# Optimization experiments

Measured on AMD Instinct MI355X. Metric: run time of the kernel, lower is better.

The kernel has to match this reference:

```python
import jax, jax.numpy as jnp
import numpy as np

B, N, HID, NH = 16, 200, 64, 2
D = HID // NH
EPS = 1e-12
LOG_EPS = 1e-24


def setup_inputs() -> dict:
    key = jax.random.key(0)
    ks = jax.random.split(key, 24)
    r = lambda k, shp, s=1.0: (jax.random.normal(k, shp, dtype=jnp.float32) * s)
    inp = {
        "input_tensor": r(ks[0], (B, N, HID), 0.5),
        "attention_mask": jnp.zeros((B, 1, N, N), jnp.float32),
        "absolute_pos_K": r(ks[1], (B, N, HID), 0.5),
        "absolute_pos_V": r(ks[2], (B, N, HID), 0.5),
        "time_matrix_emb_K": r(ks[3], (B, N, N, HID), 0.1),
        "time_matrix_emb_V": r(ks[4], (B, N, N, HID), 0.1),
        # learned params (torch nn.Linear convention: y = x @ W.T + b)
        "Wq": r(ks[5], (HID, HID), 0.02), "bq": jnp.zeros((HID,), jnp.float32),
        "Wk": r(ks[6], (HID, HID), 0.02), "bk": jnp.zeros((HID,), jnp.float32),
        "Wv": r(ks[7], (HID, HID), 0.02), "bv": jnp.zeros((HID,), jnp.float32),
        "Wd": r(ks[8], (HID, HID), 0.02), "bd": jnp.zeros((HID,), jnp.float32),
        "order_w": r(ks[9], (2 * D,), 0.02), "order_b": jnp.zeros((1,), jnp.float32),
        "dist_w": r(ks[10], (2 * D,), 0.02), "dist_b": jnp.zeros((1,), jnp.float32),
        "scalar": r(ks[11], (1,)),
        "ln_g": jnp.ones((HID,), jnp.float32), "ln_b": jnp.zeros((HID,), jnp.float32),
    }
    return inp


def _split_heads(x):  # [B,N,HID] -> [B,NH,N,D]
    return x.reshape(B, N, NH, D).transpose(0, 2, 1, 3)


def reference(input_tensor, attention_mask, absolute_pos_K, absolute_pos_V,
              time_matrix_emb_K, time_matrix_emb_V,
              Wq, bq, Wk, bk, Wv, bv, Wd, bd,
              order_w, order_b, dist_w, dist_b, scalar, ln_g, ln_b):
    q = _split_heads(input_tensor @ Wq.T + bq)   # [B,H,N,D]
    k = _split_heads(input_tensor @ Wk.T + bk)
    v = _split_heads(input_tensor @ Wv.T + bv)
    pk = _split_heads(absolute_pos_K)
    pv = _split_heads(absolute_pos_V)
    tk = time_matrix_emb_K.reshape(B, N, N, NH, D).transpose(0, 3, 1, 2, 4)  # [B,H,N,N,D]
    tv = time_matrix_emb_V.reshape(B, N, N, NH, D).transpose(0, 3, 1, 2, 4)

    scores = jnp.einsum('bhid,bhjd->bhij', q, k)
    scores = scores + jnp.einsum('bhid,bhjd->bhij', q, pk)
    scores = scores + jnp.einsum('bhijd,bhid->bhij', tk, q)

    # order term: order_affine(cat(q_i, k_j)) decomposes as q_i.w1 + k_j.w2 + b,
    # so we never materialize the [B,H,N,N,2D] q_k tensor.
    logit_o = (jnp.einsum('bhid,d->bhi', q, order_w[:D])[..., :, None]
               + jnp.einsum('bhjd,d->bhj', k, order_w[D:])[..., None, :]
               + order_b[0])
    pr_order = jax.nn.sigmoid(logit_o)
    gd_order = jnp.triu(jnp.ones((N, N), jnp.float32), 1)  # 1 where j > i
    err_order = (jnp.log(pr_order + LOG_EPS) * gd_order
                 + jnp.log(1.0 - pr_order + LOG_EPS) * (1.0 - gd_order))

    # distance term (same decomposition)
    pr_dist = (jnp.einsum('bhid,d->bhi', q, dist_w[:D])[..., :, None]
               + jnp.einsum('bhjd,d->bhj', k, dist_w[D:])[..., None, :]
               + dist_b[0])
    idx = jnp.arange(N)
    gd_dist = jnp.log(jnp.abs(idx[None, :] - idx[:, None]).astype(jnp.float32) + 1.0)
    err_dist = -jnp.square(gd_dist - pr_dist) * jnp.square(scalar[0]) * 0.5

    scores = (scores + err_order + err_dist) / np.sqrt(D).astype(np.float32)
    scores = scores + attention_mask
    probs = jax.nn.softmax(scores, axis=-1)  # dropout is identity in eval mode

    ctx = (jnp.einsum('bhij,bhjd->bhid', probs, v)
           + jnp.einsum('bhij,bhjd->bhid', probs, pv)
           + jnp.einsum('bhij,bhijd->bhid', probs, tv))
    ctx = ctx.transpose(0, 2, 1, 3).reshape(B, N, HID)

    h = ctx @ Wd.T + bd + input_tensor
    mu = h.mean(-1, keepdims=True)
    var = jnp.square(h - mu).mean(-1, keepdims=True)
    return (h - mu) / jnp.sqrt(var + EPS) * ln_g + ln_b
```

## Files before the change

kernel.cpp:

```cpp
#include <hip/hip_runtime.h>
#include <math.h>

#define B 16
#define N 200
#define HID 64
#define NH 2
#define D 32
#define EPSF 1e-12f
#define LOG_EPSF 1e-24f

#define RSQRT_D 0.17677669529663687f

__global__ __launch_bounds__(256) void k_proj(
    const float* __restrict__ x,
    const float* __restrict__ pk,
    const float* __restrict__ pv,
    const float* __restrict__ Wq, const float* __restrict__ bq,
    const float* __restrict__ Wk, const float* __restrict__ bk,
    const float* __restrict__ Wv, const float* __restrict__ bv,
    const float* __restrict__ order_w, const float* __restrict__ dist_w,
    float* __restrict__ q,
    float* __restrict__ kp,
    float* __restrict__ vp,
    float* __restrict__ qo, float* __restrict__ ko,
    float* __restrict__ qd, float* __restrict__ kd)
{
    __shared__ float sX[4][HID];
    const int tid = threadIdx.x;
    const int sub = tid >> 6;
    const int o   = tid & 63;
    const int row = blockIdx.x * 4 + sub;

    sX[sub][o] = x[row * HID + o];
    __syncthreads();

    float qv = bq[o], kv = bk[o], vv = bv[o];
    #pragma unroll 8
    for (int c = 0; c < HID; ++c) {
        const float xv = sX[sub][c];
        qv = fmaf(xv, Wq[o * HID + c], qv);
        kv = fmaf(xv, Wk[o * HID + c], kv);
        vv = fmaf(xv, Wv[o * HID + c], vv);
    }
    q [row * HID + o] = qv;
    kp[row * HID + o] = kv + pk[row * HID + o];
    vp[row * HID + o] = vv + pv[row * HID + o];

    const int d = o & 31;
    float qov = qv * order_w[d];
    float kov = kv * order_w[D + d];
    float qdv = qv * dist_w[d];
    float kdv = kv * dist_w[D + d];
    #pragma unroll
    for (int m = 16; m >= 1; m >>= 1) {
        qov += __shfl_xor(qov, m);
        kov += __shfl_xor(kov, m);
        qdv += __shfl_xor(qdv, m);
        kdv += __shfl_xor(kdv, m);
    }
    if (d == 0) {
        const int bb = row / N;
        const int ii = row - bb * N;
        const int h  = o >> 5;
        const int idx = (bb * NH + h) * N + ii;
        qo[idx] = qov;  ko[idx] = kov;
        qd[idx] = qdv;  kd[idx] = kdv;
    }
}

__global__ __launch_bounds__(64) void k_attn(
    const float* __restrict__ q, const float* __restrict__ kp,
    const float* __restrict__ vp,
    const float* __restrict__ tk,
    const float* __restrict__ tv,
    const float* __restrict__ amask,
    const float* __restrict__ qo, const float* __restrict__ ko,
    const float* __restrict__ qd, const float* __restrict__ kd,
    const float* __restrict__ order_b, const float* __restrict__ dist_b,
    const float* __restrict__ scalar,
    float* __restrict__ ctx)
{
    __shared__ float S_aux[256];
    __shared__ float S_dot[256];

    const int lane = threadIdx.x;
    const int g    = lane >> 3;
    const int c    = lane & 7;
    const int bid  = blockIdx.x;
    const int bh   = bid / N;
    const int i    = bid - bh * N;
    const int b    = bh >> 1;
    const int h    = bh & 1;
    const int bi   = b * N + i;

    const float4 qf = ((const float4*)(q + (size_t)bi * HID + h * D))[c];

    const float qoi = qo[bh * N + i];
    const float qdi = qd[bh * N + i];
    const float ob  = order_b[0];
    const float db  = dist_b[0];
    const float sc  = scalar[0];
    const float sc2h = 0.5f * sc * sc;

    const float* kpb = kp + (size_t)b * N * HID + h * D;
    const float* tkb = tk + (size_t)bi * N * HID + h * D;
    const float* vpb = vp + (size_t)b * N * HID + h * D;
    const float* tvb = tv + (size_t)bi * N * HID + h * D;
    const float* mb  = amask + (size_t)bi * N;
    const float* kob = ko + (size_t)bh * N;
    const float* kdb = kd + (size_t)bh * N;

    #pragma unroll
    for (int r = 0; r < 4; ++r) {
        const int j = r * 64 + lane;
        if (j < N) {
            const float lo = qoi + kob[j] + ob;
            const float xs = (j > i) ? -lo : lo;
            const float eo = -log1pf(expf(xs));
            const float pd = qdi + kdb[j] + db;
            const float gd = logf((float)(j > i ? j - i : i - j) + 1.0f);
            const float dv = gd - pd;
            S_aux[j] = (eo - sc2h * dv * dv) * RSQRT_D + mb[j];
        }
    }

    #pragma unroll 5
    for (int it = 0; it < 25; ++it) {
        const int j = it * 8 + g;
        const float4 kv  = ((const float4*)(kpb + (size_t)j * HID))[c];
        const float4 tkv = ((const float4*)(tkb + (size_t)j * HID))[c];
        float part = qf.x * (kv.x + tkv.x) + qf.y * (kv.y + tkv.y)
                   + qf.z * (kv.z + tkv.z) + qf.w * (kv.w + tkv.w);
        part += __shfl_xor(part, 1);
        part += __shfl_xor(part, 2);
        part += __shfl_xor(part, 4);
        if (c == 0) S_dot[j] = part * RSQRT_D;
    }
    asm volatile("s_waitcnt lgkmcnt(0)" ::: "memory");

    const float s0 = S_aux[lane]       + S_dot[lane];
    const float s1 = S_aux[lane + 64]  + S_dot[lane + 64];
    const float s2 = S_aux[lane + 128] + S_dot[lane + 128];
    const float s3 = (lane < 8) ? (S_aux[lane + 192] + S_dot[lane + 192]) : -INFINITY;
    float m = fmaxf(fmaxf(s0, s1), fmaxf(s2, s3));
    #pragma unroll
    for (int k = 32; k >= 1; k >>= 1) m = fmaxf(m, __shfl_xor(m, k));
    const float e0 = expf(s0 - m);
    const float e1 = expf(s1 - m);
    const float e2 = expf(s2 - m);
    const float e3 = (lane < 8) ? expf(s3 - m) : 0.0f;
    float t = e0 + e1 + e2 + e3;
    #pragma unroll
    for (int k = 32; k >= 1; k >>= 1) t += __shfl_xor(t, k);
    const float rinv = 1.0f / t;
    S_aux[lane]       = e0 * rinv;
    S_aux[lane + 64]  = e1 * rinv;
    S_aux[lane + 128] = e2 * rinv;
    if (lane < 8) S_aux[lane + 192] = e3 * rinv;
    asm volatile("s_waitcnt lgkmcnt(0)" ::: "memory");

    float4 r4 = make_float4(0.f, 0.f, 0.f, 0.f);
    #pragma unroll 5
    for (int it = 0; it < 25; ++it) {
        const int j = it * 8 + g;
        const float p = S_aux[j];
        const float4 vv  = ((const float4*)(vpb + (size_t)j * HID))[c];
        const float4 tvv = ((const float4*)(tvb + (size_t)j * HID))[c];
        r4.x += p * (vv.x + tvv.x);
        r4.y += p * (vv.y + tvv.y);
        r4.z += p * (vv.z + tvv.z);
        r4.w += p * (vv.w + tvv.w);
    }
    #pragma unroll
    for (int k = 8; k <= 32; k <<= 1) {
        r4.x += __shfl_xor(r4.x, k);
        r4.y += __shfl_xor(r4.y, k);
        r4.z += __shfl_xor(r4.z, k);
        r4.w += __shfl_xor(r4.w, k);
    }
    if (g == 0)
        ((float4*)(ctx + (size_t)bi * HID + h * D))[c] = r4;
}

__global__ __launch_bounds__(256) void k_out(
    const float* __restrict__ ctx, const float* __restrict__ x,
    const float* __restrict__ Wd, const float* __restrict__ bd,
    const float* __restrict__ ln_g, const float* __restrict__ ln_b,
    float* __restrict__ out)
{
    __shared__ float sC[4][HID];
    const int tid = threadIdx.x;
    const int sub = tid >> 6;
    const int o   = tid & 63;
    const int row = blockIdx.x * 4 + sub;

    sC[sub][o] = ctx[row * HID + o];
    __syncthreads();

    float hv = bd[o] + x[row * HID + o];
    #pragma unroll 8
    for (int c = 0; c < HID; ++c)
        hv = fmaf(sC[sub][c], Wd[o * HID + c], hv);

    float sum = hv;
    #pragma unroll
    for (int m = 32; m >= 1; m >>= 1) sum += __shfl_xor(sum, m);
    const float mu = sum * (1.0f / 64.0f);
    const float dv = hv - mu;
    float vs = dv * dv;
    #pragma unroll
    for (int m = 32; m >= 1; m >>= 1) vs += __shfl_xor(vs, m);
    const float var = vs * (1.0f / 64.0f);

    out[row * HID + o] = dv * rsqrtf(var + EPSF) * ln_g[o] + ln_b[o];
}

extern "C" void kernel_launch(void* const* d_in, const int* in_sizes, int n_in,
                              void* d_out, int out_size, void* d_ws, size_t ws_size,
                              hipStream_t stream) {
    const float* x     = (const float*)d_in[0];
    const float* amask = (const float*)d_in[1];
    const float* apk   = (const float*)d_in[2];
    const float* apv   = (const float*)d_in[3];
    const float* tk    = (const float*)d_in[4];
    const float* tv    = (const float*)d_in[5];
    const float* Wq    = (const float*)d_in[6];
    const float* bq    = (const float*)d_in[7];
    const float* Wk    = (const float*)d_in[8];
    const float* bk    = (const float*)d_in[9];
    const float* Wv    = (const float*)d_in[10];
    const float* bv    = (const float*)d_in[11];
    const float* Wd    = (const float*)d_in[12];
    const float* bd    = (const float*)d_in[13];
    const float* order_w = (const float*)d_in[14];
    const float* order_b = (const float*)d_in[15];
    const float* dist_w  = (const float*)d_in[16];
    const float* dist_b  = (const float*)d_in[17];
    const float* scalar  = (const float*)d_in[18];
    const float* ln_g    = (const float*)d_in[19];
    const float* ln_b    = (const float*)d_in[20];

    float* ws = (float*)d_ws;
    const size_t nrow = (size_t)B * N * HID;
    float* qbuf  = ws;
    float* kpbuf = ws + nrow;
    float* vpbuf = ws + 2 * nrow;
    float* ctxb  = ws + 3 * nrow;
    float* qob   = ws + 4 * nrow;
    float* kob   = qob + (size_t)B * NH * N;
    float* qdb   = kob + (size_t)B * NH * N;
    float* kdb   = qdb + (size_t)B * NH * N;

    k_proj<<<(B * N) / 4, 256, 0, stream>>>(x, apk, apv, Wq, bq, Wk, bk, Wv, bv,
                                            order_w, dist_w,
                                            qbuf, kpbuf, vpbuf, qob, kob, qdb, kdb);

    k_attn<<<B * NH * N, 64, 0, stream>>>(qbuf, kpbuf, vpbuf, tk, tv, amask,
                                          qob, kob, qdb, kdb,
                                          order_b, dist_b, scalar, ctxb);

    k_out<<<(B * N) / 4, 256, 0, stream>>>(ctxb, x, Wd, bd, ln_g, ln_b,
                                           (float*)d_out);
}
```

Measured before the change: 106.7 us.

## Restructure attention kernel to process both heads per row with contiguous loads

```diff
diff --git a/kernel.cpp b/kernel.cpp
--- a/kernel.cpp
+++ b/kernel.cpp
@@ -10,6 +10,15 @@
 #define LOG_EPSF 1e-24f
 
 #define RSQRT_D 0.17677669529663687f
+
+__device__ __forceinline__ float dpp_qperm_add(float x, const int ctrl) {
+    int yi;
+    switch (ctrl) {
+        case 0xB1: yi = __builtin_amdgcn_mov_dpp(__float_as_int(x), 0xB1, 0xF, 0xF, true); break;
+        default:   yi = __builtin_amdgcn_mov_dpp(__float_as_int(x), 0x4E, 0xF, 0xF, true); break;
+    }
+    return x + __int_as_float(yi);
+}
 
 __global__ __launch_bounds__(256) void k_proj(
     const float* __restrict__ x,
@@ -68,7 +77,7 @@
     }
 }
 
-__global__ __launch_bounds__(64) void k_attn(
+__global__ __launch_bounds__(128, 6) void k_attn(
     const float* __restrict__ q, const float* __restrict__ kp,
     const float* __restrict__ vp,
     const float* __restrict__ tk,
@@ -80,106 +89,123 @@
     const float* __restrict__ scalar,
     float* __restrict__ ctx)
 {
-    __shared__ float S_aux[256];
-    __shared__ float S_dot[256];
-
-    const int lane = threadIdx.x;
-    const int g    = lane >> 3;
-    const int c    = lane & 7;
-    const int bid  = blockIdx.x;
-    const int bh   = bid / N;
-    const int i    = bid - bh * N;
-    const int b    = bh >> 1;
-    const int h    = bh & 1;
-    const int bi   = b * N + i;
-
-    const float4 qf = ((const float4*)(q + (size_t)bi * HID + h * D))[c];
-
-    const float qoi = qo[bh * N + i];
-    const float qdi = qd[bh * N + i];
+    __shared__ float  W2[1024];
+    __shared__ float  SA[512];
+    __shared__ float  SP[512];
+    __shared__ float4 CP[128];
+
+    const int tid  = threadIdx.x;
+    const int w    = tid >> 6;
+    const int lane = tid & 63;
+    const int jj   = lane >> 4;
+    const int c    = lane & 15;
+    const int head = c >> 3;
+    const int p    = (c >> 2) & 1;
+
+    const int bi = blockIdx.x;
+    const int b  = bi / N;
+    const int i  = bi - b * N;
+
+    const float* qoB = qo + (size_t)(2 * b) * N;
+    const float* koB = ko + (size_t)(2 * b) * N;
+    const float* qdB = qd + (size_t)(2 * b) * N;
+    const float* kdB = kd + (size_t)(2 * b) * N;
     const float ob  = order_b[0];
     const float db  = dist_b[0];
     const float sc  = scalar[0];
     const float sc2h = 0.5f * sc * sc;
-
-    const float* kpb = kp + (size_t)b * N * HID + h * D;
-    const float* tkb = tk + (size_t)bi * N * HID + h * D;
-    const float* vpb = vp + (size_t)b * N * HID + h * D;
-    const float* tvb = tv + (size_t)bi * N * HID + h * D;
+    const float qoi0 = qoB[i],       qoi1 = qoB[N + i];
+    const float qdi0 = qdB[i],       qdi1 = qdB[N + i];
     const float* mb  = amask + (size_t)bi * N;
-    const float* kob = ko + (size_t)bh * N;
-    const float* kdb = kd + (size_t)bh * N;
+
+    float4 qf = ((const float4*)(q + (size_t)bi * HID))[c];
+    qf.x *= RSQRT_D; qf.y *= RSQRT_D; qf.z *= RSQRT_D; qf.w *= RSQRT_D;
+
+    const float4* kpR = (const float4*)(kp + ((size_t)b * N + w * 100) * HID);
+    const float4* tkR = (const float4*)(tk + (((size_t)b * N + i) * N + w * 100) * HID);
+    const float4* vpR = (const float4*)(vp + ((size_t)b * N + w * 100) * HID);
+    const float4* tvR = (const float4*)(tv + (((size_t)b * N + i) * N + w * 100) * HID);
 
     #pragma unroll
     for (int r = 0; r < 4; ++r) {
-        const int j = r * 64 + lane;
-        if (j < N) {
-            const float lo = qoi + kob[j] + ob;
+        const int e = tid + 128 * r;
+        if (e < 2 * N) {
+            const int h = (e >= N);
+            const int j = e - (h ? N : 0);
+            const float lo = (h ? qoi1 : qoi0) + koB[e] + ob;
             const float xs = (j > i) ? -lo : lo;
             const float eo = -log1pf(expf(xs));
-            const float pd = qdi + kdb[j] + db;
+            const float pd = (h ? qdi1 : qdi0) + kdB[e] + db;
             const float gd = logf((float)(j > i ? j - i : i - j) + 1.0f);
             const float dv = gd - pd;
-            S_aux[j] = (eo - sc2h * dv * dv) * RSQRT_D + mb[j];
+            SA[h * 256 + j] = (eo - sc2h * dv * dv) * RSQRT_D + mb[j];
         }
     }
 
-    #pragma unroll 5
+    const int wbase = p * 520 + head * 272 + w * 100 + jj;
+    #pragma unroll
     for (int it = 0; it < 25; ++it) {
-        const int j = it * 8 + g;
-        const float4 kv  = ((const float4*)(kpb + (size_t)j * HID))[c];
-        const float4 tkv = ((const float4*)(tkb + (size_t)j * HID))[c];
+        const float4 kv  = kpR[it * 64 + lane];
+        const float4 tkv = tkR[it * 64 + lane];
         float part = qf.x * (kv.x + tkv.x) + qf.y * (kv.y + tkv.y)
                    + qf.z * (kv.z + tkv.z) + qf.w * (kv.w + tkv.w);
-        part += __shfl_xor(part, 1);
-        part += __shfl_xor(part, 2);
-        part += __shfl_xor(part, 4);
-        if (c == 0) S_dot[j] = part * RSQRT_D;
-    }
-    asm volatile("s_waitcnt lgkmcnt(0)" ::: "memory");
-
-    const float s0 = S_aux[lane]       + S_dot[lane];
-    const float s1 = S_aux[lane + 64]  + S_dot[lane + 64];
-    const float s2 = S_aux[lane + 128] + S_dot[lane + 128];
-    const float s3 = (lane < 8) ? (S_aux[lane + 192] + S_dot[lane + 192]) : -INFINITY;
-    float m = fmaxf(fmaxf(s0, s1), fmaxf(s2, s3));
-    #pragma unroll
-    for (int k = 32; k >= 1; k >>= 1) m = fmaxf(m, __shfl_xor(m, k));
-    const float e0 = expf(s0 - m);
-    const float e1 = expf(s1 - m);
-    const float e2 = expf(s2 - m);
-    const float e3 = (lane < 8) ? expf(s3 - m) : 0.0f;
-    float t = e0 + e1 + e2 + e3;
-    #pragma unroll
-    for (int k = 32; k >= 1; k >>= 1) t += __shfl_xor(t, k);
-    const float rinv = 1.0f / t;
-    S_aux[lane]       = e0 * rinv;
-    S_aux[lane + 64]  = e1 * rinv;
-    S_aux[lane + 128] = e2 * rinv;
-    if (lane < 8) S_aux[lane + 192] = e3 * rinv;
-    asm volatile("s_waitcnt lgkmcnt(0)" ::: "memory");
-
-    float4 r4 = make_float4(0.f, 0.f, 0.f, 0.f);
-    #pragma unroll 5
+        part = dpp_qperm_add(part, 0xB1);
+        part = dpp_qperm_add(part, 0x4E);
+        if ((lane & 3) == 0)
+            W2[wbase + it * 4] = part;
+    }
+    __syncthreads();
+
+    {
+        const int hb272 = w * 272;
+        const int hb256 = w * 256;
+        const float s0 = W2[hb272 + lane]       + W2[520 + hb272 + lane]       + SA[hb256 + lane];
+        const float s1 = W2[hb272 + lane + 64]  + W2[520 + hb272 + lane + 64]  + SA[hb256 + lane + 64];
+        const float s2 = W2[hb272 + lane + 128] + W2[520 + hb272 + lane + 128] + SA[hb256 + lane + 128];
+        const float s3 = (lane < 8) ? (W2[hb272 + lane + 192] + W2[520 + hb272 + lane + 192]
+                                       + SA[hb256 + lane + 192]) : -INFINITY;
+        float m = fmaxf(fmaxf(s0, s1), fmaxf(s2, s3));
+        #pragma unroll
+        for (int k = 32; k >= 1; k >>= 1) m = fmaxf(m, __shfl_xor(m, k));
+        const float e0 = expf(s0 - m);
+        const float e1 = expf(s1 - m);
+        const float e2 = expf(s2 - m);
+        const float e3 = (lane < 8) ? expf(s3 - m) : 0.0f;
+        float t = e0 + e1 + e2 + e3;
+        #pragma unroll
+        for (int k = 32; k >= 1; k >>= 1) t += __shfl_xor(t, k);
+        const float rinv = 1.0f / t;
+        SP[hb256 + lane]       = e0 * rinv;
+        SP[hb256 + lane + 64]  = e1 * rinv;
+        SP[hb256 + lane + 128] = e2 * rinv;
+        if (lane < 8) SP[hb256 + lane + 192] = e3 * rinv;
+    }
+    __syncthreads();
+
+    float4 acc = make_float4(0.f, 0.f, 0.f, 0.f);
+    const int pbase = head * 256 + w * 100 + jj;
+    #pragma unroll
     for (int it = 0; it < 25; ++it) {
-        const int j = it * 8 + g;
-        const float p = S_aux[j];
-        const float4 vv  = ((const float4*)(vpb + (size_t)j * HID))[c];
-        const float4 tvv = ((const float4*)(tvb + (size_t)j * HID))[c];
-        r4.x += p * (vv.x + tvv.x);
-        r4.y += p * (vv.y + tvv.y);
-        r4.z += p * (vv.z + tvv.z);
-        r4.w += p * (vv.w + tvv.w);
-    }
-    #pragma unroll
-    for (int k = 8; k <= 32; k <<= 1) {
-        r4.x += __shfl_xor(r4.x, k);
-        r4.y += __shfl_xor(r4.y, k);
-        r4.z += __shfl_xor(r4.z, k);
-        r4.w += __shfl_xor(r4.w, k);
-    }
-    if (g == 0)
-        ((float4*)(ctx + (size_t)bi * HID + h * D))[c] = r4;
+        const float pj = SP[pbase + it * 4];
+        const float4 vv = vpR[it * 64 + lane];
+        const float4 tt = tvR[it * 64 + lane];
+        acc.x = fmaf(pj, vv.x + tt.x, acc.x);
+        acc.y = fmaf(pj, vv.y + tt.y, acc.y);
+        acc.z = fmaf(pj, vv.z + tt.z, acc.z);
+        acc.w = fmaf(pj, vv.w + tt.w, acc.w);
+    }
+    CP[tid] = acc;
+    __syncthreads();
+
+    if (tid < 16) {
+        float4 s = CP[tid];
+        #pragma unroll
+        for (int g = 1; g < 8; ++g) {
+            const float4 t4 = CP[g * 16 + tid];
+            s.x += t4.x; s.y += t4.y; s.z += t4.z; s.w += t4.w;
+        }
+        ((float4*)(ctx + (size_t)bi * HID))[tid] = s;
+    }
 }
 
 __global__ __launch_bounds__(256) void k_out(
@@ -255,9 +281,9 @@
                                             order_w, dist_w,
                                             qbuf, kpbuf, vpbuf, qob, kob, qdb, kdb);
 
-    k_attn<<<B * NH * N, 64, 0, stream>>>(qbuf, kpbuf, vpbuf, tk, tv, amask,
-                                          qob, kob, qdb, kdb,
-                                          order_b, dist_b, scalar, ctxb);
+    k_attn<<<B * N, 128, 0, stream>>>(qbuf, kpbuf, vpbuf, tk, tv, amask,
+                                      qob, kob, qdb, kdb,
+                                      order_b, dist_b, scalar, ctxb);
 
     k_out<<<(B * N) / 4, 256, 0, stream>>>(ctxb, x, Wd, bd, ln_g, ln_b,
                                            (float*)d_out);
```

Result: slower. 139.5 us (+30.8%).

## Split attention into precompute, time-embedding streaming, and tiled PV kernels

Applied to the files above, without the earlier changes.

```diff
diff --git a/kernel.cpp b/kernel.cpp
--- a/kernel.cpp
+++ b/kernel.cpp
@@ -7,7 +7,6 @@
 #define NH 2
 #define D 32
 #define EPSF 1e-12f
-#define LOG_EPSF 1e-24f
 
 #define RSQRT_D 0.17677669529663687f
 
@@ -68,20 +67,82 @@
     }
 }
 
-__global__ __launch_bounds__(64) void k_attn(
+__global__ __launch_bounds__(256) void k_pre(
     const float* __restrict__ q, const float* __restrict__ kp,
-    const float* __restrict__ vp,
-    const float* __restrict__ tk,
-    const float* __restrict__ tv,
     const float* __restrict__ amask,
     const float* __restrict__ qo, const float* __restrict__ ko,
     const float* __restrict__ qd, const float* __restrict__ kd,
     const float* __restrict__ order_b, const float* __restrict__ dist_b,
     const float* __restrict__ scalar,
-    float* __restrict__ ctx)
-{
-    __shared__ float S_aux[256];
+    float* __restrict__ S_pre)
+{
+    __shared__ float sQ[25][33];
+    __shared__ float sK[200][33];
+    __shared__ float sGd[200];
+    __shared__ float sQo[25], sQd[25];
+    __shared__ float sKo[200], sKd[200];
+
+    const int tid = threadIdx.x;
+    const int bid = blockIdx.x;
+    const int it  = bid & 7;
+    const int bh  = bid >> 3;
+    const int b   = bh >> 1;
+    const int h   = bh & 1;
+    const int i0  = it * 25;
+
+    for (int e = tid; e < 200 * 32; e += 256) {
+        const int j = e >> 5, d = e & 31;
+        sK[j][d] = kp[((size_t)b * N + j) * HID + h * D + d];
+    }
+    for (int e = tid; e < 25 * 32; e += 256) {
+        const int ii = e >> 5, d = e & 31;
+        sQ[ii][d] = q[((size_t)b * N + i0 + ii) * HID + h * D + d];
+    }
+    for (int e = tid; e < 200; e += 256) {
+        sGd[e] = logf((float)e + 1.0f);
+        sKo[e] = ko[(size_t)bh * N + e];
+        sKd[e] = kd[(size_t)bh * N + e];
+    }
+    if (tid < 25) {
+        sQo[tid] = qo[(size_t)bh * N + i0 + tid];
+        sQd[tid] = qd[(size_t)bh * N + i0 + tid];
+    }
+    const float ob = order_b[0];
+    const float db = dist_b[0];
+    const float sc = scalar[0];
+    const float sc2h = 0.5f * sc * sc;
+    __syncthreads();
+
+    for (int e = tid; e < 25 * 200; e += 256) {
+        const int ii = e / 200;
+        const int jj = e - ii * 200;
+        const int i  = i0 + ii;
+        float dot = 0.0f;
+        #pragma unroll
+        for (int d = 0; d < 32; ++d)
+            dot = fmaf(sQ[ii][d], sK[jj][d], dot);
+        const float lo = sQo[ii] + sKo[jj] + ob;
+        const float xs = (jj > i) ? -lo : lo;
+        const float eo = -log1pf(expf(xs));
+        const float pd = sQd[ii] + sKd[jj] + db;
+        const int   ad = (jj > i) ? (jj - i) : (i - jj);
+        const float dv = sGd[ad] - pd;
+        const float ed = -sc2h * dv * dv;
+        S_pre[((size_t)bh * N + i) * N + jj] =
+            (dot + eo + ed) * RSQRT_D + amask[((size_t)b * N + i) * N + jj];
+    }
+}
+
+__global__ __launch_bounds__(64) void k_attn(
+    const float* __restrict__ q,
+    const float* __restrict__ tk,
+    const float* __restrict__ tv,
+    const float* __restrict__ S_pre,
+    float* __restrict__ P,
+    float* __restrict__ ctx_tv)
+{
     __shared__ float S_dot[256];
+    __shared__ float SP[256];
 
     const int lane = threadIdx.x;
     const int g    = lane >> 3;
@@ -93,55 +154,36 @@
     const int h    = bh & 1;
     const int bi   = b * N + i;
 
-    const float4 qf = ((const float4*)(q + (size_t)bi * HID + h * D))[c];
-
-    const float qoi = qo[bh * N + i];
-    const float qdi = qd[bh * N + i];
-    const float ob  = order_b[0];
-    const float db  = dist_b[0];
-    const float sc  = scalar[0];
-    const float sc2h = 0.5f * sc * sc;
-
-    const float* kpb = kp + (size_t)b * N * HID + h * D;
-    const float* tkb = tk + (size_t)bi * N * HID + h * D;
-    const float* vpb = vp + (size_t)b * N * HID + h * D;
-    const float* tvb = tv + (size_t)bi * N * HID + h * D;
-    const float* mb  = amask + (size_t)bi * N;
-    const float* kob = ko + (size_t)bh * N;
-    const float* kdb = kd + (size_t)bh * N;
-
-    #pragma unroll
-    for (int r = 0; r < 4; ++r) {
-        const int j = r * 64 + lane;
-        if (j < N) {
-            const float lo = qoi + kob[j] + ob;
-            const float xs = (j > i) ? -lo : lo;
-            const float eo = -log1pf(expf(xs));
-            const float pd = qdi + kdb[j] + db;
-            const float gd = logf((float)(j > i ? j - i : i - j) + 1.0f);
-            const float dv = gd - pd;
-            S_aux[j] = (eo - sc2h * dv * dv) * RSQRT_D + mb[j];
-        }
-    }
-
-    #pragma unroll 5
+    float4 qf = ((const float4*)(q + (size_t)bi * HID + h * D))[c];
+    qf.x *= RSQRT_D; qf.y *= RSQRT_D; qf.z *= RSQRT_D; qf.w *= RSQRT_D;
+
+    const float4* tkR = (const float4*)(tk + ((size_t)bi * N) * HID + h * D);
+    const float4* tvR = (const float4*)(tv + ((size_t)bi * N) * HID + h * D);
+    const float*  spr = S_pre + ((size_t)bh * N + i) * N;
+
+    const float sp0 = spr[lane];
+    const float sp1 = spr[lane + 64];
+    const float sp2 = spr[lane + 128];
+    const float sp3 = (lane < 8) ? spr[lane + 192] : 0.0f;
+
+    float4 cur = tkR[(size_t)g * 16 + c];
+    #pragma unroll
     for (int it = 0; it < 25; ++it) {
-        const int j = it * 8 + g;
-        const float4 kv  = ((const float4*)(kpb + (size_t)j * HID))[c];
-        const float4 tkv = ((const float4*)(tkb + (size_t)j * HID))[c];
-        float part = qf.x * (kv.x + tkv.x) + qf.y * (kv.y + tkv.y)
-                   + qf.z * (kv.z + tkv.z) + qf.w * (kv.w + tkv.w);
+        float4 nxt;
+        if (it < 24) nxt = tkR[(size_t)((it + 1) * 8 + g) * 16 + c];
+        float part = qf.x * cur.x + qf.y * cur.y + qf.z * cur.z + qf.w * cur.w;
         part += __shfl_xor(part, 1);
         part += __shfl_xor(part, 2);
         part += __shfl_xor(part, 4);
-        if (c == 0) S_dot[j] = part * RSQRT_D;
+        if (c == 0) S_dot[it * 8 + g] = part;
+        cur = nxt;
     }
     asm volatile("s_waitcnt lgkmcnt(0)" ::: "memory");
 
-    const float s0 = S_aux[lane]       + S_dot[lane];
-    const float s1 = S_aux[lane + 64]  + S_dot[lane + 64];
-    const float s2 = S_aux[lane + 128] + S_dot[lane + 128];
-    const float s3 = (lane < 8) ? (S_aux[lane + 192] + S_dot[lane + 192]) : -INFINITY;
+    const float s0 = sp0 + S_dot[lane];
+    const float s1 = sp1 + S_dot[lane + 64];
+    const float s2 = sp2 + S_dot[lane + 128];
+    const float s3 = (lane < 8) ? (sp3 + S_dot[lane + 192]) : -INFINITY;
     float m = fmaxf(fmaxf(s0, s1), fmaxf(s2, s3));
     #pragma unroll
     for (int k = 32; k >= 1; k >>= 1) m = fmaxf(m, __shfl_xor(m, k));
@@ -153,37 +195,77 @@
     #pragma unroll
     for (int k = 32; k >= 1; k >>= 1) t += __shfl_xor(t, k);
     const float rinv = 1.0f / t;
-    S_aux[lane]       = e0 * rinv;
-    S_aux[lane + 64]  = e1 * rinv;
-    S_aux[lane + 128] = e2 * rinv;
-    if (lane < 8) S_aux[lane + 192] = e3 * rinv;
+    const float p0 = e0 * rinv, p1 = e1 * rinv, p2 = e2 * rinv, p3 = e3 * rinv;
+    SP[lane]       = p0;
+    SP[lane + 64]  = p1;
+    SP[lane + 128] = p2;
+    if (lane < 8) SP[lane + 192] = p3;
+
+    float* prow = P + ((size_t)bh * N + i) * N;
+    prow[lane]       = p0;
+    prow[lane + 64]  = p1;
+    prow[lane + 128] = p2;
+    if (lane < 8) prow[lane + 192] = p3;
+
     asm volatile("s_waitcnt lgkmcnt(0)" ::: "memory");
 
-    float4 r4 = make_float4(0.f, 0.f, 0.f, 0.f);
-    #pragma unroll 5
+    float4 acc = make_float4(0.f, 0.f, 0.f, 0.f);
+    float4 cv = tvR[(size_t)g * 16 + c];
+    #pragma unroll
     for (int it = 0; it < 25; ++it) {
-        const int j = it * 8 + g;
-        const float p = S_aux[j];
-        const float4 vv  = ((const float4*)(vpb + (size_t)j * HID))[c];
-        const float4 tvv = ((const float4*)(tvb + (size_t)j * HID))[c];
-        r4.x += p * (vv.x + tvv.x);
-        r4.y += p * (vv.y + tvv.y);
-        r4.z += p * (vv.z + tvv.z);
-        r4.w += p * (vv.w + tvv.w);
+        float4 nv;
+        if (it < 24) nv = tvR[(size_t)((it + 1) * 8 + g) * 16 + c];
+        const float pj = SP[it * 8 + g];
+        acc.x = fmaf(pj, cv.x, acc.x);
+        acc.y = fmaf(pj, cv.y, acc.y);
+        acc.z = fmaf(pj, cv.z, acc.z);
+        acc.w = fmaf(pj, cv.w, acc.w);
+        cv = nv;
     }
     #pragma unroll
     for (int k = 8; k <= 32; k <<= 1) {
-        r4.x += __shfl_xor(r4.x, k);
-        r4.y += __shfl_xor(r4.y, k);
-        r4.z += __shfl_xor(r4.z, k);
-        r4.w += __shfl_xor(r4.w, k);
+        acc.x += __shfl_xor(acc.x, k);
+        acc.y += __shfl_xor(acc.y, k);
+        acc.z += __shfl_xor(acc.z, k);
+        acc.w += __shfl_xor(acc.w, k);
     }
     if (g == 0)
-        ((float4*)(ctx + (size_t)bi * HID + h * D))[c] = r4;
+        ((float4*)(ctx_tv + (size_t)bi * HID + h * D))[c] = acc;
+}
+
+__global__ __launch_bounds__(256) void k_pv(
+    const float* __restrict__ P, const float* __restrict__ vp,
+    float* __restrict__ ctx_vp)
+{
+    __shared__ float sV[200][33];
+    const int tid = threadIdx.x;
+    const int bid = blockIdx.x;
+    const int it  = bid & 7;
+    const int bh  = bid >> 3;
+    const int b   = bh >> 1;
+    const int h   = bh & 1;
+    const int i0  = it * 25;
+
+    for (int e = tid; e < 200 * 32; e += 256) {
+        const int j = e >> 5, d = e & 31;
+        sV[j][d] = vp[((size_t)b * N + j) * HID + h * D + d];
+    }
+    __syncthreads();
+
+    for (int e = tid; e < 25 * 32; e += 256) {
+        const int ii = e >> 5, d = e & 31;
+        const float* pr = P + ((size_t)bh * N + i0 + ii) * N;
+        float acc = 0.0f;
+        #pragma unroll 8
+        for (int j = 0; j < 200; ++j)
+            acc = fmaf(pr[j], sV[j][d], acc);
+        ctx_vp[((size_t)bh * N + i0 + ii) * D + d] = acc;
+    }
 }
 
 __global__ __launch_bounds__(256) void k_out(
-    const float* __restrict__ ctx, const float* __restrict__ x,
+    const float* __restrict__ ctx_tv, const float* __restrict__ ctx_vp,
+    const float* __restrict__ x,
     const float* __restrict__ Wd, const float* __restrict__ bd,
     const float* __restrict__ ln_g, const float* __restrict__ ln_b,
     float* __restrict__ out)
@@ -193,11 +275,15 @@
     const int sub = tid >> 6;
     const int o   = tid & 63;
     const int row = blockIdx.x * 4 + sub;
-
-    sC[sub][o] = ctx[row * HID + o];
+    const int b   = row / N;
+    const int i   = row - b * N;
+    const int h   = o >> 5;
+
+    sC[sub][o] = ctx_tv[(size_t)row * HID + o]
+               + ctx_vp[((size_t)(b * NH + h) * N + i) * D + (o & 31)];
     __syncthreads();
 
-    float hv = bd[o] + x[row * HID + o];
+    float hv = bd[o] + x[(size_t)row * HID + o];
     #pragma unroll 8
     for (int c = 0; c < HID; ++c)
         hv = fmaf(sC[sub][c], Wd[o * HID + c], hv);
@@ -212,7 +298,7 @@
     for (int m = 32; m >= 1; m >>= 1) vs += __shfl_xor(vs, m);
     const float var = vs * (1.0f / 64.0f);
 
-    out[row * HID + o] = dv * rsqrtf(var + EPSF) * ln_g[o] + ln_b[o];
+    out[(size_t)row * HID + o] = dv * rsqrtf(var + EPSF) * ln_g[o] + ln_b[o];
 }
 
 extern "C" void kernel_launch(void* const* d_in, const int* in_sizes, int n_in,
@@ -242,23 +328,30 @@
 
     float* ws = (float*)d_ws;
     const size_t nrow = (size_t)B * N * HID;
-    float* qbuf  = ws;
-    float* kpbuf = ws + nrow;
-    float* vpbuf = ws + 2 * nrow;
-    float* ctxb  = ws + 3 * nrow;
-    float* qob   = ws + 4 * nrow;
-    float* kob   = qob + (size_t)B * NH * N;
-    float* qdb   = kob + (size_t)B * NH * N;
-    float* kdb   = qdb + (size_t)B * NH * N;
+    const size_t nbh  = (size_t)B * NH * N;
+    float* qbuf   = ws;
+    float* kpbuf  = qbuf  + nrow;
+    float* vpbuf  = kpbuf + nrow;
+    float* ctxtv  = vpbuf + nrow;
+    float* ctxvp  = ctxtv + nrow;
+    float* qob    = ctxvp + (size_t)nbh * D;
+    float* kob    = qob + nbh;
+    float* qdb    = kob + nbh;
+    float* kdb    = qdb + nbh;
+    float* Spre   = kdb + nbh;
+    float* Pbuf   = Spre + (size_t)nbh * N;
 
     k_proj<<<(B * N) / 4, 256, 0, stream>>>(x, apk, apv, Wq, bq, Wk, bk, Wv, bv,
                                             order_w, dist_w,
                                             qbuf, kpbuf, vpbuf, qob, kob, qdb, kdb);
 
-    k_attn<<<B * NH * N, 64, 0, stream>>>(qbuf, kpbuf, vpbuf, tk, tv, amask,
-                                          qob, kob, qdb, kdb,
-                                          order_b, dist_b, scalar, ctxb);
-
-    k_out<<<(B * N) / 4, 256, 0, stream>>>(ctxb, x, Wd, bd, ln_g, ln_b,
+    k_pre<<<B * NH * 8, 256, 0, stream>>>(qbuf, kpbuf, amask, qob, kob, qdb, kdb,
+                                          order_b, dist_b, scalar, Spre);
+
+    k_attn<<<B * NH * N, 64, 0, stream>>>(qbuf, tk, tv, Spre, Pbuf, ctxtv);
+
+    k_pv<<<B * NH * 8, 256, 0, stream>>>(Pbuf, vpbuf, ctxvp);
+
+    k_out<<<(B * N) / 4, 256, 0, stream>>>(ctxtv, ctxvp, x, Wd, bd, ln_g, ln_b,
                                            (float*)d_out);
 }
```

New measurement: 151.0 us. +41.5%, slower.
